# Performance work log

Measured on AMD Instinct MI355X. Metric: run time of the kernel, lower is better.

Reference implementation:

```python
import jax, jax.numpy as jnp
import numpy as np

N_GENES = 15135
K = int(np.ceil(0.5 * N_GENES))  # 7568, PyG TopKPooling ratio=0.5
BS, E, F_IN, H, HF, NC, L = 8, 242160, 64, 128, 512, 2, 3


def setup_inputs() -> dict:
    key = jax.random.key(0)
    ks = jax.random.split(key, 16)
    def lin(k, fin, fout):
        s = 1.0 / np.sqrt(fin)
        return jax.random.normal(k, (fin, fout), jnp.float32) * s
    x = jax.random.normal(ks[0], (BS, N_GENES, F_IN), jnp.float32)
    batch = jnp.zeros((BS,), jnp.int32)
    edge_index = jax.random.randint(ks[1], (2, E), 0, N_GENES, dtype=jnp.int32)
    CAT = L * H
    return {
        "x": x,
        "batch": batch,
        "edge_index": edge_index,
        "W1": lin(ks[2], F_IN, H), "b1": jnp.zeros((H,), jnp.float32),
        "W2": lin(ks[3], H, H),    "b2": jnp.zeros((H,), jnp.float32),
        "W3": lin(ks[4], H, H),    "b3": jnp.zeros((H,), jnp.float32),
        "topk_w": jax.random.normal(ks[5], (CAT,), jnp.float32) / np.sqrt(CAT),
        "fcW": lin(ks[6], CAT, 1), "fcb": jnp.zeros((1,), jnp.float32),
        "lin1W": lin(ks[7], K, HF), "lin1b": jnp.zeros((HF,), jnp.float32),
        "lin2W": lin(ks[8], HF, NC), "lin2b": jnp.zeros((NC,), jnp.float32),
    }


def reference(x, batch, edge_index, W1, b1, W2, b2, W3, b3,
              topk_w, fcW, fcb, lin1W, lin1b, lin2W, lin2b):
    bs = x.shape[0]
    # --- GCN normalization with self-loops (PyG GCNConv defaults) ---
    loop = jnp.arange(N_GENES, dtype=edge_index.dtype)
    src = jnp.concatenate([edge_index[0], loop])
    dst = jnp.concatenate([edge_index[1], loop])
    deg = jnp.zeros((N_GENES,), x.dtype).at[dst].add(1.0)
    dinv = jax.lax.rsqrt(deg)  # deg >= 1 due to self-loops
    norm = dinv[src] * dinv[dst]  # [E+N]

    def gcn(h, W, b):
        h = h @ W                                   # [bs, N, H]
        msg = h[:, src, :] * norm[None, :, None]    # gather + edge weight
        agg = jnp.zeros_like(h).at[:, dst, :].add(msg)  # scatter-add
        return agg + b

    h1 = jax.nn.relu(gcn(x, W1, b1))
    h2 = jax.nn.relu(gcn(h1, W2, b2))
    h3 = jax.nn.relu(gcn(h2, W3, b3))
    # mode='cat': stack on last dim then flatten -> feature order (H, layer)
    xc = jnp.stack([h1, h2, h3], -1).reshape(bs, N_GENES, -1)  # [bs, N, L*H]

    # --- TopKPooling (score = tanh(x.w/||w||), keep top ceil(0.5*N)) ---
    score = jnp.tanh((xc @ topk_w) / jnp.linalg.norm(topk_w))  # [bs, N]
    top_s, perm = jax.lax.top_k(score, K)                       # [bs, K]
    xp = jnp.take_along_axis(xc, perm[..., None], axis=1) * top_s[..., None]

    z = (xp @ fcW + fcb)[..., 0]          # [bs, K]
    h = jax.nn.relu(z @ lin1W + lin1b)    # [bs, HF]; dropout inactive (eval)
    logits = h @ lin2W + lin2b            # [bs, NC]
    return jax.nn.log_softmax(logits, axis=-1)
```

## Files before the change

kernel.cpp:

```cpp
#include <hip/hip_runtime.h>

#define N_G   15135
#define E_N   242160
#define BSZ   8
#define K_TOP 7568
#define NH    128
#define NBIN  65536
#define SUFS  65600

typedef float f4v __attribute__((ext_vector_type(4)));

__global__ void zero_kernel(int* __restrict__ p, int n) {
  int i = blockIdx.x * 1024 + threadIdx.x;
  if (i < n) p[i] = 0;
}

__global__ void count_kernel(const int* __restrict__ ei, int* __restrict__ cnt) {
  int e = blockIdx.x * 256 + threadIdx.x;
  if (e < E_N) atomicAdd(&cnt[ei[E_N + e]], 1);
}

__global__ __launch_bounds__(1024) void scan_kernel(const int* __restrict__ cnt,
                                                    int* __restrict__ rowstart,
                                                    float* __restrict__ dinv,
                                                    int4* __restrict__ rowdesc,
                                                    int* __restrict__ gctr,
                                                    const float* __restrict__ topk_w,
                                                    float* __restrict__ scal) {
  __shared__ int buf[1024];
  __shared__ int base;
  int tid = threadIdx.x;
  int i = blockIdx.x * 1024 + tid;
  int v = (i < N_G) ? cnt[i] : 0;
  float di = 1.0f / sqrtf((float)(v + 1));
  if (i < N_G) dinv[i] = di;
  buf[tid] = v;
  __syncthreads();
  for (int s = 1; s < 1024; s <<= 1) {
    int t = (tid >= s) ? buf[tid - s] : 0;
    __syncthreads();
    buf[tid] += t;
    __syncthreads();
  }
  if (tid == 1023) base = atomicAdd(gctr, buf[1023]);
  __syncthreads();
  if (i < N_G) {
    int rs = base + buf[tid] - v;
    rowstart[i] = rs;
    rowdesc[i] = make_int4(rs, v, __float_as_int(di), 0);
  }
  if (blockIdx.x == 0) {
    __shared__ float fbuf[512];
    if (tid < 512) {
      float w = (tid < 384) ? topk_w[tid] : 0.f;
      fbuf[tid] = w * w;
    }
    __syncthreads();
    for (int s = 256; s > 0; s >>= 1) {
      if (tid < s) fbuf[tid] += fbuf[tid + s];
      __syncthreads();
    }
    if (tid == 0) scal[0] = 1.0f / sqrtf(fbuf[0]);
  }
}

__global__ void fill_kernel(const int* __restrict__ ei, const int* __restrict__ rowstart,
                            const float* __restrict__ dinv, int* __restrict__ fillc,
                            int2* __restrict__ csr) {
  int e = blockIdx.x * 256 + threadIdx.x;
  if (e < E_N) {
    int s = ei[e], d = ei[E_N + e];
    int pos = rowstart[d] + atomicAdd(&fillc[d], 1);
    csr[pos] = make_int2(s, __float_as_int(dinv[s]));
  }
}

template<int CIN, bool BR>
__global__ __launch_bounds__(256, 6) void mm_kernel(const float* __restrict__ A,
                                                    const float* __restrict__ W,
                                                    const float* __restrict__ bias,
                                                    float* __restrict__ out) {
  __shared__ float Bst[32][132];
  __shared__ float Ast2[32][68];
  int tid = threadIdx.x;
  int b = blockIdx.x & 7;
  int ib = blockIdx.x >> 3;
  int rb0 = b * N_G + ib * 64;
  int rmax = N_G - ib * 64;
  int c0 = (tid & 31) * 4;
  int r0 = (tid >> 5) * 8;
  float acc[8][4];
#pragma unroll
  for (int i = 0; i < 8; i++)
#pragma unroll
    for (int j = 0; j < 4; j++) acc[i][j] = 0.f;

  for (int k0 = 0; k0 < CIN; k0 += 32) {
    {
      int koff = (tid & 7) * 4;
      int row = tid >> 3;
#pragma unroll
      for (int p = 0; p < 2; ++p) {
        int r = row + p * 32;
        f4v v = {0.f, 0.f, 0.f, 0.f};
        if (r < rmax) v = __builtin_nontemporal_load((const f4v*)(A + (size_t)(rb0 + r) * CIN + k0 + koff));
        Ast2[koff + 0][r] = v.x; Ast2[koff + 1][r] = v.y;
        Ast2[koff + 2][r] = v.z; Ast2[koff + 3][r] = v.w;
      }
    }
    {
      int cc = (tid & 31) * 4;
      int kr = tid >> 5;
#pragma unroll
      for (int p = 0; p < 4; ++p) {
        int k = kr + p * 8;
        *(float4*)&Bst[k][cc] = *(const float4*)(W + (size_t)(k0 + k) * NH + cc);
      }
    }
    __syncthreads();
#pragma unroll 4
    for (int kk = 0; kk < 32; ++kk) {
      float a[8], bb[4];
      *(float4*)&a[0] = *(const float4*)&Ast2[kk][r0];
      *(float4*)&a[4] = *(const float4*)&Ast2[kk][r0 + 4];
      *(float4*)&bb[0] = *(const float4*)&Bst[kk][c0];
#pragma unroll
      for (int i = 0; i < 8; i++)
#pragma unroll
        for (int j = 0; j < 4; j++)
          acc[i][j] = fmaf(a[i], bb[j], acc[i][j]);
    }
    __syncthreads();
  }
  float b0 = 0.f, b1 = 0.f, b2 = 0.f, b3 = 0.f;
  if (BR) { b0 = bias[c0]; b1 = bias[c0+1]; b2 = bias[c0+2]; b3 = bias[c0+3]; }
#pragma unroll
  for (int i = 0; i < 8; i++) {
    int r = r0 + i;
    if (r < rmax) {
      float4 v;
      if (BR) {
        v.x = fmaxf(acc[i][0] + b0, 0.f); v.y = fmaxf(acc[i][1] + b1, 0.f);
        v.z = fmaxf(acc[i][2] + b2, 0.f); v.w = fmaxf(acc[i][3] + b3, 0.f);
      } else {
        v.x = acc[i][0]; v.y = acc[i][1]; v.z = acc[i][2]; v.w = acc[i][3];
      }
      *(float4*)(out + (size_t)(rb0 + r) * NH + c0) = v;
    }
  }
}

template<int CH, bool BR>
__global__ __launch_bounds__(256) void agg_h_kernel(const float* __restrict__ src,
                                                    const int2* __restrict__ csr,
                                                    const int4* __restrict__ rowdesc,
                                                    const float* __restrict__ bias,
                                                    float* __restrict__ dst, int half) {
  int b = blockIdx.x & 7;
  int chunk = blockIdx.x >> 3;
  int wave = threadIdx.x >> 6, lane = threadIdx.x & 63;
  int d = chunk * 4 + wave;
  if (d >= N_G) return;
  d = __builtin_amdgcn_readfirstlane(d);
  int4 rd = rowdesc[d];
  int e0 = rd.x, n = rd.y;
  float dv = __int_as_float(rd.z);
  int c = (CH == 128) ? ((half << 6) + lane) : lane;
  const float* sb = src + (size_t)b * N_G * CH;
  const int2* ce = csr + e0;
  float acc[8];
  acc[0] = dv * sb[(size_t)d * CH + c];
#pragma unroll
  for (int k = 1; k < 8; ++k) acc[k] = 0.f;
  int l = 0;
  if (n >= 8) {
    int2 pA[8]; float vA[8];
#pragma unroll
    for (int k = 0; k < 8; ++k) pA[k] = ce[k];
#pragma unroll
    for (int k = 0; k < 8; ++k) vA[k] = sb[(size_t)pA[k].x * CH + c];
    l = 8;
    for (; l + 8 <= n; l += 8) {
      int2 pB[8]; float vB[8];
#pragma unroll
      for (int k = 0; k < 8; ++k) pB[k] = ce[l + k];
#pragma unroll
      for (int k = 0; k < 8; ++k) vB[k] = sb[(size_t)pB[k].x * CH + c];
#pragma unroll
      for (int k = 0; k < 8; ++k) acc[k] = fmaf(__int_as_float(pA[k].y), vA[k], acc[k]);
#pragma unroll
      for (int k = 0; k < 8; ++k) { pA[k] = pB[k]; vA[k] = vB[k]; }
    }
#pragma unroll
    for (int k = 0; k < 8; ++k) acc[k] = fmaf(__int_as_float(pA[k].y), vA[k], acc[k]);
  }
  for (; l < n; ++l) {
    int2 p = ce[l];
    acc[0] = fmaf(__int_as_float(p.y), sb[(size_t)p.x * CH + c], acc[0]);
  }
  float s = ((acc[0] + acc[1]) + (acc[2] + acc[3])) + ((acc[4] + acc[5]) + (acc[6] + acc[7]));
  float r = BR ? fmaxf(fmaf(dv, s, bias[c]), 0.f) : dv * s;
  __builtin_nontemporal_store(r, &dst[((size_t)b * N_G + d) * CH + c]);
}

__global__ __launch_bounds__(256) void agg_score_h_kernel(const float* __restrict__ hw,
                                                          const int2* __restrict__ csr,
                                                          const int4* __restrict__ rowdesc,
                                                          const float* __restrict__ bias,
                                                          const float* __restrict__ h1,
                                                          const float* __restrict__ h2,
                                                          const float* __restrict__ topk_w,
                                                          const float* __restrict__ fcW,
                                                          float* __restrict__ pd1,
                                                          float* __restrict__ pd2, int half) {
  int b = blockIdx.x & 7;
  int chunk = blockIdx.x >> 3;
  int wave = threadIdx.x >> 6, lane = threadIdx.x & 63;
  int d = chunk * 4 + wave;
  if (d >= N_G) return;
  d = __builtin_amdgcn_readfirstlane(d);
  int4 rd = rowdesc[d];
  int e0 = rd.x, n = rd.y;
  float dv = __int_as_float(rd.z);
  int c = (half << 6) + lane;
  const float* sb = hw + (size_t)b * N_G * NH;
  const int2* ce = csr + e0;
  size_t rbase = ((size_t)b * N_G + d) * NH + c;
  float u1 = __builtin_nontemporal_load(h1 + rbase);
  float u2 = __builtin_nontemporal_load(h2 + rbase);
  float acc[8];
  acc[0] = dv * sb[(size_t)d * NH + c];
#pragma unroll
  for (int k = 1; k < 8; ++k) acc[k] = 0.f;
  int l = 0;
  if (n >= 8) {
    int2 pA[8]; float vA[8];
#pragma unroll
    for (int k = 0; k < 8; ++k) pA[k] = ce[k];
#pragma unroll
    for (int k = 0; k < 8; ++k) vA[k] = sb[(size_t)pA[k].x * NH + c];
    l = 8;
    for (; l + 8 <= n; l += 8) {
      int2 pB[8]; float vB[8];
#pragma unroll
      for (int k = 0; k < 8; ++k) pB[k] = ce[l + k];
#pragma unroll
      for (int k = 0; k < 8; ++k) vB[k] = sb[(size_t)pB[k].x * NH + c];
#pragma unroll
      for (int k = 0; k < 8; ++k) acc[k] = fmaf(__int_as_float(pA[k].y), vA[k], acc[k]);
#pragma unroll
      for (int k = 0; k < 8; ++k) { pA[k] = pB[k]; vA[k] = vB[k]; }
    }
#pragma unroll
    for (int k = 0; k < 8; ++k) acc[k] = fmaf(__int_as_float(pA[k].y), vA[k], acc[k]);
  }
  for (; l < n; ++l) {
    int2 p = ce[l];
    acc[0] = fmaf(__int_as_float(p.y), sb[(size_t)p.x * NH + c], acc[0]);
  }
  float s = ((acc[0] + acc[1]) + (acc[2] + acc[3])) + ((acc[4] + acc[5]) + (acc[6] + acc[7]));
  float r = fmaxf(fmaf(dv, s, bias[c]), 0.f);
  float d1 = u1 * topk_w[c * 3] + u2 * topk_w[c * 3 + 1] + r * topk_w[c * 3 + 2];
  float d2 = u1 * fcW[c * 3]    + u2 * fcW[c * 3 + 1]    + r * fcW[c * 3 + 2];
#pragma unroll
  for (int sh = 32; sh > 0; sh >>= 1) {
    d1 += __shfl_down(d1, sh);
    d2 += __shfl_down(d2, sh);
  }
  if (lane == 0) {
    int gw = b * N_G + d;
    pd1[gw * 2 + half] = d1;
    pd2[gw * 2 + half] = d2;
  }
}

__global__ void combine_kernel(const float* __restrict__ pd1, const float* __restrict__ pd2,
                               const float* __restrict__ scal, float* __restrict__ score,
                               float* __restrict__ d2a, unsigned* __restrict__ keys,
                               int* __restrict__ hist) {
  int b = blockIdx.y;
  int i = blockIdx.x * 256 + threadIdx.x;
  if (i >= N_G) return;
  int gw = b * N_G + i;
  float d1 = pd1[2 * gw] + pd1[2 * gw + 1];
  float d2 = pd2[2 * gw] + pd2[2 * gw + 1];
  float sc = tanhf(d1 * scal[0]);
  score[gw] = sc;
  d2a[gw] = d2;
  unsigned u = __float_as_uint(sc);
  unsigned k32 = (u & 0x80000000u) ? ~u : (u | 0x80000000u);
  keys[gw] = k32;
  atomicAdd(&hist[b * NBIN + (int)(k32 >> 16)], 1);
}

__global__ __launch_bounds__(1024) void suffix_kernel(const int* __restrict__ hist,
                                                      int* __restrict__ suf) {
  __shared__ int buf[1024];
  int b = blockIdx.x;
  const int* hb = hist + b * NBIN;
  int* sb = suf + b * SUFS;
  int t = threadIdx.x;
  int base = t * 64;
  int s = 0;
  for (int k = 0; k < 64; ++k) s += hb[base + k];
  buf[t] = s;
  __syncthreads();
  for (int off = 1; off < 1024; off <<= 1) {
    int v = (t + off < 1024) ? buf[t + off] : 0;
    __syncthreads();
    buf[t] += v;
    __syncthreads();
  }
  int acc = buf[t] - s;
  if (t == 0) sb[NBIN] = 0;
  for (int k = 63; k >= 0; --k) {
    acc += hb[base + k];
    sb[base + k] = acc;
  }
}

__global__ void scatter_kernel(const unsigned* __restrict__ keys, int* __restrict__ hist,
                               const int* __restrict__ suf, int2* __restrict__ bucket) {
  int b = blockIdx.y;
  int i = blockIdx.x * 256 + threadIdx.x;
  if (i >= N_G) return;
  unsigned k = keys[b * N_G + i];
  int bin = (int)(k >> 16);
  int old = atomicSub(&hist[b * NBIN + bin], 1);
  int pos = suf[b * SUFS + bin + 1] + old - 1;
  bucket[b * N_G + pos] = make_int2((int)k, i);
}

__global__ void rank_z_kernel(const unsigned* __restrict__ keys, const int* __restrict__ suf,
                              const int2* __restrict__ bucket, const float* __restrict__ score,
                              const float* __restrict__ d2a, const float* __restrict__ fcb,
                              float* __restrict__ z) {
  int b = blockIdx.y;
  int i = blockIdx.x * 256 + threadIdx.x;
  if (i >= N_G) return;
  int gw = b * N_G + i;
  unsigned k = keys[gw];
  int bin = (int)(k >> 16);
  int lo = suf[b * SUFS + bin + 1];
  int hi = suf[b * SUFS + bin];
  int r = lo;
  const int2* bk = bucket + b * N_G;
  for (int p = lo; p < hi; ++p) {
    int2 e = bk[p];
    unsigned kj = (unsigned)e.x;
    r += (kj > k || (kj == k && e.y < i)) ? 1 : 0;
  }
  if (r < K_TOP) z[b * K_TOP + r] = fmaf(score[gw], d2a[gw], fcb[0]);
}

__global__ __launch_bounds__(256) void lin1_kernel(const float* __restrict__ z,
                                                   const float* __restrict__ W,
                                                   float* __restrict__ hpre) {
  __shared__ float zb[237];
  int b = blockIdx.y, rs = blockIdx.x;
  int r0 = rs * 237;
  int rn = K_TOP - r0; if (rn > 237) rn = 237;
  for (int q = threadIdx.x; q < rn; q += 256) zb[q] = z[b * K_TOP + r0 + q];
  __syncthreads();
  int c = threadIdx.x;
  float a0 = 0.f, a1 = 0.f;
  for (int r = 0; r < rn; ++r) {
    float zz = zb[r];
    const float* wr = W + (size_t)(r0 + r) * 512;
    a0 = fmaf(zz, wr[c], a0);
    a1 = fmaf(zz, wr[c + 256], a1);
  }
  atomicAdd(&hpre[b * 512 + c], a0);
  atomicAdd(&hpre[b * 512 + c + 256], a1);
}

__global__ __launch_bounds__(128) void lin2_kernel(const float* __restrict__ hpre,
                                                   const float* __restrict__ l1b,
                                                   const float* __restrict__ W2,
                                                   const float* __restrict__ l2b,
                                                   float* __restrict__ out) {
  int b = blockIdx.x, tid = threadIdx.x;
  float a0 = 0.f, a1 = 0.f;
  for (int j = tid; j < 512; j += 128) {
    float t = fmaxf(hpre[b * 512 + j] + l1b[j], 0.f);
    a0 = fmaf(t, W2[j * 2 + 0], a0);
    a1 = fmaf(t, W2[j * 2 + 1], a1);
  }
#pragma unroll
  for (int s = 32; s > 0; s >>= 1) {
    a0 += __shfl_down(a0, s);
    a1 += __shfl_down(a1, s);
  }
  __shared__ float red[2][2];
  if ((tid & 63) == 0) { red[tid >> 6][0] = a0; red[tid >> 6][1] = a1; }
  __syncthreads();
  if (tid == 0) {
    float l0 = red[0][0] + red[1][0] + l2b[0];
    float l1 = red[0][1] + red[1][1] + l2b[1];
    float m = fmaxf(l0, l1);
    float lse = m + logf(expf(l0 - m) + expf(l1 - m));
    out[b * 2 + 0] = l0 - lse;
    out[b * 2 + 1] = l1 - lse;
  }
}

extern "C" void kernel_launch(void* const* d_in, const int* in_sizes, int n_in,
                              void* d_out, int out_size, void* d_ws, size_t ws_size,
                              hipStream_t stream) {
  const float* x   = (const float*)d_in[0];
  const int*   ei  = (const int*)d_in[2];
  const float* W1  = (const float*)d_in[3];
  const float* b1  = (const float*)d_in[4];
  const float* W2  = (const float*)d_in[5];
  const float* b2  = (const float*)d_in[6];
  const float* W3  = (const float*)d_in[7];
  const float* b3  = (const float*)d_in[8];
  const float* tkw = (const float*)d_in[9];
  const float* fcW = (const float*)d_in[10];
  const float* fcb = (const float*)d_in[11];
  const float* l1W = (const float*)d_in[12];
  const float* l1b = (const float*)d_in[13];
  const float* l2W = (const float*)d_in[14];
  const float* l2b = (const float*)d_in[15];
  float* out = (float*)d_out;

  char* ws = (char*)d_ws;
  size_t off = 0;
  auto alloc = [&](size_t bytes) {
    char* p = ws + off;
    off += (bytes + 255) & ~(size_t)255;
    return p;
  };
  int*   cnt   = (int*)alloc(15136 * 4);
  int*   fillc = (int*)alloc(15136 * 4);
  int*   gctr  = (int*)alloc(256);
  float* hpre  = (float*)alloc(4096 * 4);
  int*   hist  = (int*)alloc((size_t)BSZ * NBIN * 4);
  int*   rowstart = (int*)alloc(15136 * 4);
  float* dinv  = (float*)alloc(15136 * 4);
  int4*  rowdesc = (int4*)alloc(15136 * 16);
  float* scal  = (float*)alloc(64);
  float* z     = (float*)alloc((size_t)BSZ * K_TOP * 4);
  float* score = (float*)alloc(121088 * 4);
  float* d2a   = (float*)alloc(121088 * 4);
  unsigned* keys = (unsigned*)alloc(121088 * 4);
  int*   suf   = (int*)alloc((size_t)BSZ * SUFS * 4);
  int2*  bucket = (int2*)alloc(121088 * 8);
  float* pd1   = (float*)alloc(121088 * 2 * 4);
  float* pd2   = (float*)alloc(121088 * 2 * 4);
  int2*  csr   = (int2*)alloc((size_t)E_N * 8);
  float* ax = (float*)alloc((size_t)BSZ * N_G * 64 * 4);
  float* hw = (float*)alloc((size_t)BSZ * N_G * NH * 4);
  float* h1 = (float*)alloc((size_t)BSZ * N_G * NH * 4);
  float* h2 = (float*)alloc((size_t)BSZ * N_G * NH * 4);
  (void)ws_size; (void)in_sizes; (void)n_in; (void)out_size;

  int zero_n = (int)(((char*)rowstart - (char*)cnt) / 4);
  zero_kernel<<<(zero_n + 1023) / 1024, 1024, 0, stream>>>(cnt, zero_n);
  count_kernel<<<(E_N + 255) / 256, 256, 0, stream>>>(ei, cnt);
  scan_kernel<<<(N_G + 1023) / 1024, 1024, 0, stream>>>(cnt, rowstart, dinv, rowdesc, gctr, tkw, scal);
  fill_kernel<<<(E_N + 255) / 256, 256, 0, stream>>>(ei, rowstart, dinv, fillc, csr);

  dim3 mmg(8 * 237);
  int aggblocks = 8 * ((N_G + 3) / 4);

  agg_h_kernel<64, false><<<aggblocks, 256, 0, stream>>>(x, csr, rowdesc, nullptr, ax, 0);
  mm_kernel<64, true><<<mmg, 256, 0, stream>>>(ax, W1, b1, h1);
  mm_kernel<128, false><<<mmg, 256, 0, stream>>>(h1, W2, nullptr, hw);
  agg_h_kernel<128, true><<<aggblocks, 256, 0, stream>>>(hw, csr, rowdesc, b2, h2, 0);
  agg_h_kernel<128, true><<<aggblocks, 256, 0, stream>>>(hw, csr, rowdesc, b2, h2, 1);
  mm_kernel<128, false><<<mmg, 256, 0, stream>>>(h2, W3, nullptr, hw);
  agg_score_h_kernel<<<aggblocks, 256, 0, stream>>>(hw, csr, rowdesc, b3,
                                                    h1, h2, tkw, fcW, pd1, pd2, 0);
  agg_score_h_kernel<<<aggblocks, 256, 0, stream>>>(hw, csr, rowdesc, b3,
                                                    h1, h2, tkw, fcW, pd1, pd2, 1);

  dim3 ng((N_G + 255) / 256, BSZ);
  combine_kernel<<<ng, 256, 0, stream>>>(pd1, pd2, scal, score, d2a, keys, hist);
  suffix_kernel<<<BSZ, 1024, 0, stream>>>(hist, suf);
  scatter_kernel<<<ng, 256, 0, stream>>>(keys, hist, suf, bucket);
  rank_z_kernel<<<ng, 256, 0, stream>>>(keys, suf, bucket, score, d2a, fcb, z);

  dim3 l1g(32, BSZ);
  lin1_kernel<<<l1g, 256, 0, stream>>>(z, l1W, hpre);
  lin2_kernel<<<BSZ, 128, 0, stream>>>(hpre, l1b, l2W, l2b, out);
}
```

Baseline: 663.4 us.

## Merge half-channel aggregation passes into single float2 pass and fuse score combine

The 128-channel GCN aggregations previously ran as two launches, one per 64-channel half, each re-walking the CSR edge list. Now each lane gathers a float2 covering both halves in one pass, which halves the edge-index traffic and launch count and widens each gather. The score kernel also does the tanh, key and histogram work directly, so the partial-dot buffers and the combine kernel are removed. The trade-off is more registers per thread for the float2 accumulators and a different floating-point summation order.

```diff
diff --git a/kernel.cpp b/kernel.cpp
--- a/kernel.cpp
+++ b/kernel.cpp
@@ -9,6 +9,7 @@
 #define SUFS  65600
 
 typedef float f4v __attribute__((ext_vector_type(4)));
+typedef float f2v __attribute__((ext_vector_type(2)));
 
 __global__ void zero_kernel(int* __restrict__ p, int n) {
   int i = blockIdx.x * 1024 + threadIdx.x;
@@ -150,12 +151,10 @@
   }
 }
 
-template<int CH, bool BR>
-__global__ __launch_bounds__(256) void agg_h_kernel(const float* __restrict__ src,
+__global__ __launch_bounds__(256) void agg64_kernel(const float* __restrict__ src,
                                                     const int2* __restrict__ csr,
                                                     const int4* __restrict__ rowdesc,
-                                                    const float* __restrict__ bias,
-                                                    float* __restrict__ dst, int half) {
+                                                    float* __restrict__ dst) {
   int b = blockIdx.x & 7;
   int chunk = blockIdx.x >> 3;
   int wave = threadIdx.x >> 6, lane = threadIdx.x & 63;
@@ -165,11 +164,10 @@
   int4 rd = rowdesc[d];
   int e0 = rd.x, n = rd.y;
   float dv = __int_as_float(rd.z);
-  int c = (CH == 128) ? ((half << 6) + lane) : lane;
-  const float* sb = src + (size_t)b * N_G * CH;
+  const float* sb = src + (size_t)b * N_G * 64;
   const int2* ce = csr + e0;
   float acc[8];
-  acc[0] = dv * sb[(size_t)d * CH + c];
+  acc[0] = dv * sb[(size_t)d * 64 + lane];
 #pragma unroll
   for (int k = 1; k < 8; ++k) acc[k] = 0.f;
   int l = 0;
@@ -178,14 +176,14 @@
 #pragma unroll
     for (int k = 0; k < 8; ++k) pA[k] = ce[k];
 #pragma unroll
-    for (int k = 0; k < 8; ++k) vA[k] = sb[(size_t)pA[k].x * CH + c];
+    for (int k = 0; k < 8; ++k) vA[k] = sb[(size_t)pA[k].x * 64 + lane];
     l = 8;
     for (; l + 8 <= n; l += 8) {
       int2 pB[8]; float vB[8];
 #pragma unroll
       for (int k = 0; k < 8; ++k) pB[k] = ce[l + k];
 #pragma unroll
-      for (int k = 0; k < 8; ++k) vB[k] = sb[(size_t)pB[k].x * CH + c];
+      for (int k = 0; k < 8; ++k) vB[k] = sb[(size_t)pB[k].x * 64 + lane];
 #pragma unroll
       for (int k = 0; k < 8; ++k) acc[k] = fmaf(__int_as_float(pA[k].y), vA[k], acc[k]);
 #pragma unroll
@@ -196,23 +194,17 @@
   }
   for (; l < n; ++l) {
     int2 p = ce[l];
-    acc[0] = fmaf(__int_as_float(p.y), sb[(size_t)p.x * CH + c], acc[0]);
+    acc[0] = fmaf(__int_as_float(p.y), sb[(size_t)p.x * 64 + lane], acc[0]);
   }
   float s = ((acc[0] + acc[1]) + (acc[2] + acc[3])) + ((acc[4] + acc[5]) + (acc[6] + acc[7]));
-  float r = BR ? fmaxf(fmaf(dv, s, bias[c]), 0.f) : dv * s;
-  __builtin_nontemporal_store(r, &dst[((size_t)b * N_G + d) * CH + c]);
-}
-
-__global__ __launch_bounds__(256) void agg_score_h_kernel(const float* __restrict__ hw,
-                                                          const int2* __restrict__ csr,
-                                                          const int4* __restrict__ rowdesc,
-                                                          const float* __restrict__ bias,
-                                                          const float* __restrict__ h1,
-                                                          const float* __restrict__ h2,
-                                                          const float* __restrict__ topk_w,
-                                                          const float* __restrict__ fcW,
-                                                          float* __restrict__ pd1,
-                                                          float* __restrict__ pd2, int half) {
+  __builtin_nontemporal_store(dv * s, &dst[((size_t)b * N_G + d) * 64 + lane]);
+}
+
+__global__ __launch_bounds__(256) void agg_f2_kernel(const float* __restrict__ hw,
+                                                     const int2* __restrict__ csr,
+                                                     const int4* __restrict__ rowdesc,
+                                                     const float* __restrict__ bias,
+                                                     float* __restrict__ hout) {
   int b = blockIdx.x & 7;
   int chunk = blockIdx.x >> 3;
   int wave = threadIdx.x >> 6, lane = threadIdx.x & 63;
@@ -222,46 +214,141 @@
   int4 rd = rowdesc[d];
   int e0 = rd.x, n = rd.y;
   float dv = __int_as_float(rd.z);
-  int c = (half << 6) + lane;
-  const float* sb = hw + (size_t)b * N_G * NH;
+  const f2v* sb = (const f2v*)(hw + (size_t)b * N_G * NH);
   const int2* ce = csr + e0;
-  size_t rbase = ((size_t)b * N_G + d) * NH + c;
-  float u1 = __builtin_nontemporal_load(h1 + rbase);
-  float u2 = __builtin_nontemporal_load(h2 + rbase);
-  float acc[8];
-  acc[0] = dv * sb[(size_t)d * NH + c];
-#pragma unroll
-  for (int k = 1; k < 8; ++k) acc[k] = 0.f;
+  f2v self = sb[(size_t)d * 64 + lane];
+  float ax[4], ay[4];
+  ax[0] = dv * self.x; ay[0] = dv * self.y;
+#pragma unroll
+  for (int k = 1; k < 4; ++k) { ax[k] = 0.f; ay[k] = 0.f; }
   int l = 0;
   if (n >= 8) {
-    int2 pA[8]; float vA[8];
+    int2 pA[8]; f2v vA[8];
 #pragma unroll
     for (int k = 0; k < 8; ++k) pA[k] = ce[k];
 #pragma unroll
-    for (int k = 0; k < 8; ++k) vA[k] = sb[(size_t)pA[k].x * NH + c];
+    for (int k = 0; k < 8; ++k) vA[k] = sb[(size_t)pA[k].x * 64 + lane];
     l = 8;
     for (; l + 8 <= n; l += 8) {
-      int2 pB[8]; float vB[8];
+      int2 pB[8]; f2v vB[8];
 #pragma unroll
       for (int k = 0; k < 8; ++k) pB[k] = ce[l + k];
 #pragma unroll
-      for (int k = 0; k < 8; ++k) vB[k] = sb[(size_t)pB[k].x * NH + c];
-#pragma unroll
-      for (int k = 0; k < 8; ++k) acc[k] = fmaf(__int_as_float(pA[k].y), vA[k], acc[k]);
+      for (int k = 0; k < 8; ++k) vB[k] = sb[(size_t)pB[k].x * 64 + lane];
+#pragma unroll
+      for (int k = 0; k < 8; ++k) {
+        float w = __int_as_float(pA[k].y);
+        ax[k & 3] = fmaf(w, vA[k].x, ax[k & 3]);
+        ay[k & 3] = fmaf(w, vA[k].y, ay[k & 3]);
+      }
 #pragma unroll
       for (int k = 0; k < 8; ++k) { pA[k] = pB[k]; vA[k] = vB[k]; }
     }
 #pragma unroll
-    for (int k = 0; k < 8; ++k) acc[k] = fmaf(__int_as_float(pA[k].y), vA[k], acc[k]);
+    for (int k = 0; k < 8; ++k) {
+      float w = __int_as_float(pA[k].y);
+      ax[k & 3] = fmaf(w, vA[k].x, ax[k & 3]);
+      ay[k & 3] = fmaf(w, vA[k].y, ay[k & 3]);
+    }
   }
   for (; l < n; ++l) {
     int2 p = ce[l];
-    acc[0] = fmaf(__int_as_float(p.y), sb[(size_t)p.x * NH + c], acc[0]);
-  }
-  float s = ((acc[0] + acc[1]) + (acc[2] + acc[3])) + ((acc[4] + acc[5]) + (acc[6] + acc[7]));
-  float r = fmaxf(fmaf(dv, s, bias[c]), 0.f);
-  float d1 = u1 * topk_w[c * 3] + u2 * topk_w[c * 3 + 1] + r * topk_w[c * 3 + 2];
-  float d2 = u1 * fcW[c * 3]    + u2 * fcW[c * 3 + 1]    + r * fcW[c * 3 + 2];
+    f2v v = sb[(size_t)p.x * 64 + lane];
+    float w = __int_as_float(p.y);
+    ax[0] = fmaf(w, v.x, ax[0]); ay[0] = fmaf(w, v.y, ay[0]);
+  }
+  float sx = (ax[0] + ax[1]) + (ax[2] + ax[3]);
+  float sy = (ay[0] + ay[1]) + (ay[2] + ay[3]);
+  const f2v* bb2 = (const f2v*)bias;
+  f2v bb = bb2[lane];
+  f2v r;
+  r.x = fmaxf(fmaf(dv, sx, bb.x), 0.f);
+  r.y = fmaxf(fmaf(dv, sy, bb.y), 0.f);
+  __builtin_nontemporal_store(r, &((f2v*)hout)[((size_t)b * N_G + d) * 64 + lane]);
+}
+
+__global__ __launch_bounds__(256) void agg_score_f2_kernel(const float* __restrict__ hw,
+                                                           const int2* __restrict__ csr,
+                                                           const int4* __restrict__ rowdesc,
+                                                           const float* __restrict__ bias,
+                                                           const float* __restrict__ h1,
+                                                           const float* __restrict__ h2,
+                                                           const float* __restrict__ topk_w,
+                                                           const float* __restrict__ fcW,
+                                                           const float* __restrict__ scal,
+                                                           float* __restrict__ score,
+                                                           float* __restrict__ d2a,
+                                                           unsigned* __restrict__ keys,
+                                                           int* __restrict__ hist) {
+  int b = blockIdx.x & 7;
+  int chunk = blockIdx.x >> 3;
+  int wave = threadIdx.x >> 6, lane = threadIdx.x & 63;
+  int d = chunk * 4 + wave;
+  if (d >= N_G) return;
+  d = __builtin_amdgcn_readfirstlane(d);
+  int4 rd = rowdesc[d];
+  int e0 = rd.x, n = rd.y;
+  float dv = __int_as_float(rd.z);
+  const f2v* sb = (const f2v*)(hw + (size_t)b * N_G * NH);
+  const int2* ce = csr + e0;
+  size_t rbase = ((size_t)b * N_G + d) * 64 + lane;
+  f2v u1 = __builtin_nontemporal_load(&((const f2v*)h1)[rbase]);
+  f2v u2 = __builtin_nontemporal_load(&((const f2v*)h2)[rbase]);
+  f2v self = sb[(size_t)d * 64 + lane];
+  float ax[4], ay[4];
+  ax[0] = dv * self.x; ay[0] = dv * self.y;
+#pragma unroll
+  for (int k = 1; k < 4; ++k) { ax[k] = 0.f; ay[k] = 0.f; }
+  int l = 0;
+  if (n >= 8) {
+    int2 pA[8]; f2v vA[8];
+#pragma unroll
+    for (int k = 0; k < 8; ++k) pA[k] = ce[k];
+#pragma unroll
+    for (int k = 0; k < 8; ++k) vA[k] = sb[(size_t)pA[k].x * 64 + lane];
+    l = 8;
+    for (; l + 8 <= n; l += 8) {
+      int2 pB[8]; f2v vB[8];
+#pragma unroll
+      for (int k = 0; k < 8; ++k) pB[k] = ce[l + k];
+#pragma unroll
+      for (int k = 0; k < 8; ++k) vB[k] = sb[(size_t)pB[k].x * 64 + lane];
+#pragma unroll
+      for (int k = 0; k < 8; ++k) {
+        float w = __int_as_float(pA[k].y);
+        ax[k & 3] = fmaf(w, vA[k].x, ax[k & 3]);
+        ay[k & 3] = fmaf(w, vA[k].y, ay[k & 3]);
+      }
+#pragma unroll
+      for (int k = 0; k < 8; ++k) { pA[k] = pB[k]; vA[k] = vB[k]; }
+    }
+#pragma unroll
+    for (int k = 0; k < 8; ++k) {
+      float w = __int_as_float(pA[k].y);
+      ax[k & 3] = fmaf(w, vA[k].x, ax[k & 3]);
+      ay[k & 3] = fmaf(w, vA[k].y, ay[k & 3]);
+    }
+  }
+  for (; l < n; ++l) {
+    int2 p = ce[l];
+    f2v v = sb[(size_t)p.x * 64 + lane];
+    float w = __int_as_float(p.y);
+    ax[0] = fmaf(w, v.x, ax[0]); ay[0] = fmaf(w, v.y, ay[0]);
+  }
+  float sx = (ax[0] + ax[1]) + (ax[2] + ax[3]);
+  float sy = (ay[0] + ay[1]) + (ay[2] + ay[3]);
+  const f2v* bb2 = (const f2v*)bias;
+  f2v bb = bb2[lane];
+  float rx = fmaxf(fmaf(dv, sx, bb.x), 0.f);
+  float ry = fmaxf(fmaf(dv, sy, bb.y), 0.f);
+  const f2v* tw2 = (const f2v*)topk_w;
+  const f2v* fw2 = (const f2v*)fcW;
+  f2v ta = tw2[lane * 3 + 0], tb = tw2[lane * 3 + 1], tc = tw2[lane * 3 + 2];
+  f2v fa = fw2[lane * 3 + 0], fb = fw2[lane * 3 + 1], fc = fw2[lane * 3 + 2];
+  float d1 = u1.x * ta.x + u2.x * ta.y + rx * tb.x
+           + u1.y * tb.y + u2.y * tc.x + ry * tc.y;
+  float d2 = u1.x * fa.x + u2.x * fa.y + rx * fb.x
+           + u1.y * fb.y + u2.y * fc.x + ry * fc.y;
 #pragma unroll
   for (int sh = 32; sh > 0; sh >>= 1) {
     d1 += __shfl_down(d1, sh);
@@ -269,28 +356,14 @@
   }
   if (lane == 0) {
     int gw = b * N_G + d;
-    pd1[gw * 2 + half] = d1;
-    pd2[gw * 2 + half] = d2;
-  }
-}
-
-__global__ void combine_kernel(const float* __restrict__ pd1, const float* __restrict__ pd2,
-                               const float* __restrict__ scal, float* __restrict__ score,
-                               float* __restrict__ d2a, unsigned* __restrict__ keys,
-                               int* __restrict__ hist) {
-  int b = blockIdx.y;
-  int i = blockIdx.x * 256 + threadIdx.x;
-  if (i >= N_G) return;
-  int gw = b * N_G + i;
-  float d1 = pd1[2 * gw] + pd1[2 * gw + 1];
-  float d2 = pd2[2 * gw] + pd2[2 * gw + 1];
-  float sc = tanhf(d1 * scal[0]);
-  score[gw] = sc;
-  d2a[gw] = d2;
-  unsigned u = __float_as_uint(sc);
-  unsigned k32 = (u & 0x80000000u) ? ~u : (u | 0x80000000u);
-  keys[gw] = k32;
-  atomicAdd(&hist[b * NBIN + (int)(k32 >> 16)], 1);
+    float sc = tanhf(d1 * scal[0]);
+    score[gw] = sc;
+    d2a[gw] = d2;
+    unsigned u = __float_as_uint(sc);
+    unsigned k32 = (u & 0x80000000u) ? ~u : (u | 0x80000000u);
+    keys[gw] = k32;
+    atomicAdd(&hist[b * NBIN + (int)(k32 >> 16)], 1);
+  }
 }
 
 __global__ __launch_bounds__(1024) void suffix_kernel(const int* __restrict__ hist,
@@ -446,8 +519,6 @@
   unsigned* keys = (unsigned*)alloc(121088 * 4);
   int*   suf   = (int*)alloc((size_t)BSZ * SUFS * 4);
   int2*  bucket = (int2*)alloc(121088 * 8);
-  float* pd1   = (float*)alloc(121088 * 2 * 4);
-  float* pd2   = (float*)alloc(121088 * 2 * 4);
   int2*  csr   = (int2*)alloc((size_t)E_N * 8);
   float* ax = (float*)alloc((size_t)BSZ * N_G * 64 * 4);
   float* hw = (float*)alloc((size_t)BSZ * N_G * NH * 4);
@@ -464,19 +535,15 @@
   dim3 mmg(8 * 237);
   int aggblocks = 8 * ((N_G + 3) / 4);
 
-  agg_h_kernel<64, false><<<aggblocks, 256, 0, stream>>>(x, csr, rowdesc, nullptr, ax, 0);
+  agg64_kernel<<<aggblocks, 256, 0, stream>>>(x, csr, rowdesc, ax);
   mm_kernel<64, true><<<mmg, 256, 0, stream>>>(ax, W1, b1, h1);
   mm_kernel<128, false><<<mmg, 256, 0, stream>>>(h1, W2, nullptr, hw);
-  agg_h_kernel<128, true><<<aggblocks, 256, 0, stream>>>(hw, csr, rowdesc, b2, h2, 0);
-  agg_h_kernel<128, true><<<aggblocks, 256, 0, stream>>>(hw, csr, rowdesc, b2, h2, 1);
+  agg_f2_kernel<<<aggblocks, 256, 0, stream>>>(hw, csr, rowdesc, b2, h2);
   mm_kernel<128, false><<<mmg, 256, 0, stream>>>(h2, W3, nullptr, hw);
-  agg_score_h_kernel<<<aggblocks, 256, 0, stream>>>(hw, csr, rowdesc, b3,
-                                                    h1, h2, tkw, fcW, pd1, pd2, 0);
-  agg_score_h_kernel<<<aggblocks, 256, 0, stream>>>(hw, csr, rowdesc, b3,
-                                                    h1, h2, tkw, fcW, pd1, pd2, 1);
+  agg_score_f2_kernel<<<aggblocks, 256, 0, stream>>>(hw, csr, rowdesc, b3, h1, h2,
+                                                     tkw, fcW, scal, score, d2a, keys, hist);
 
   dim3 ng((N_G + 255) / 256, BSZ);
-  combine_kernel<<<ng, 256, 0, stream>>>(pd1, pd2, scal, score, d2a, keys, hist);
   suffix_kernel<<<BSZ, 1024, 0, stream>>>(hist, suf);
   scatter_kernel<<<ng, 256, 0, stream>>>(keys, hist, suf, bucket);
   rank_z_kernel<<<ng, 256, 0, stream>>>(keys, suf, bucket, score, d2a, fcb, z);
```

After: 615.1 us. 7.3% less time.

## Vectorize GCN aggregation with float4 gathers and fuse score/combine into last layer

Applied to the files above, without the earlier changes.

Rewrites the three aggregation kernels so each lane gathers a float4 and lanes split across edges (2 or 4 edges per wave step), reduced by cross-lane shuffles. The two half-column launches per 128-wide layer collapse into one, and the combine kernel is folded into the final aggregation, removing the pd1/pd2 partial buffers. The aim is fewer, wider memory transactions, fewer launches and less intermediate traffic. In exchange there is more per-edge index selection work, a cross-lane reduction, and half the lanes sitting idle during the epilogue.

```diff
diff --git a/kernel.cpp b/kernel.cpp
--- a/kernel.cpp
+++ b/kernel.cpp
@@ -150,12 +150,10 @@
   }
 }
 
-template<int CH, bool BR>
-__global__ __launch_bounds__(256) void agg_h_kernel(const float* __restrict__ src,
-                                                    const int2* __restrict__ csr,
-                                                    const int4* __restrict__ rowdesc,
-                                                    const float* __restrict__ bias,
-                                                    float* __restrict__ dst, int half) {
+__global__ __launch_bounds__(256) void agg64_f4_kernel(const float* __restrict__ src,
+                                                       const int2* __restrict__ csr,
+                                                       const int4* __restrict__ rowdesc,
+                                                       float* __restrict__ dst) {
   int b = blockIdx.x & 7;
   int chunk = blockIdx.x >> 3;
   int wave = threadIdx.x >> 6, lane = threadIdx.x & 63;
@@ -165,54 +163,77 @@
   int4 rd = rowdesc[d];
   int e0 = rd.x, n = rd.y;
   float dv = __int_as_float(rd.z);
-  int c = (CH == 128) ? ((half << 6) + lane) : lane;
-  const float* sb = src + (size_t)b * N_G * CH;
+  int eh = lane >> 4;
+  int q = lane & 15;
+  const f4v* sb = (const f4v*)(src + (size_t)b * N_G * 64);
   const int2* ce = csr + e0;
-  float acc[8];
-  acc[0] = dv * sb[(size_t)d * CH + c];
-#pragma unroll
-  for (int k = 1; k < 8; ++k) acc[k] = 0.f;
+  f4v acc0 = {0.f,0.f,0.f,0.f}, acc1 = {0.f,0.f,0.f,0.f};
+  int nfull = n >> 5;
   int l = 0;
-  if (n >= 8) {
-    int2 pA[8]; float vA[8];
-#pragma unroll
-    for (int k = 0; k < 8; ++k) pA[k] = ce[k];
-#pragma unroll
-    for (int k = 0; k < 8; ++k) vA[k] = sb[(size_t)pA[k].x * CH + c];
-    l = 8;
-    for (; l + 8 <= n; l += 8) {
-      int2 pB[8]; float vB[8];
-#pragma unroll
-      for (int k = 0; k < 8; ++k) pB[k] = ce[l + k];
-#pragma unroll
-      for (int k = 0; k < 8; ++k) vB[k] = sb[(size_t)pB[k].x * CH + c];
-#pragma unroll
-      for (int k = 0; k < 8; ++k) acc[k] = fmaf(__int_as_float(pA[k].y), vA[k], acc[k]);
-#pragma unroll
-      for (int k = 0; k < 8; ++k) { pA[k] = pB[k]; vA[k] = vB[k]; }
-    }
-#pragma unroll
-    for (int k = 0; k < 8; ++k) acc[k] = fmaf(__int_as_float(pA[k].y), vA[k], acc[k]);
-  }
-  for (; l < n; ++l) {
-    int2 p = ce[l];
-    acc[0] = fmaf(__int_as_float(p.y), sb[(size_t)p.x * CH + c], acc[0]);
-  }
-  float s = ((acc[0] + acc[1]) + (acc[2] + acc[3])) + ((acc[4] + acc[5]) + (acc[6] + acc[7]));
-  float r = BR ? fmaxf(fmaf(dv, s, bias[c]), 0.f) : dv * s;
-  __builtin_nontemporal_store(r, &dst[((size_t)b * N_G + d) * CH + c]);
-}
-
-__global__ __launch_bounds__(256) void agg_score_h_kernel(const float* __restrict__ hw,
-                                                          const int2* __restrict__ csr,
-                                                          const int4* __restrict__ rowdesc,
-                                                          const float* __restrict__ bias,
-                                                          const float* __restrict__ h1,
-                                                          const float* __restrict__ h2,
-                                                          const float* __restrict__ topk_w,
-                                                          const float* __restrict__ fcW,
-                                                          float* __restrict__ pd1,
-                                                          float* __restrict__ pd2, int half) {
+  for (int blk = 0; blk < nfull; ++blk, l += 32) {
+    int srcs[8]; float ws[8];
+#pragma unroll
+    for (int k = 0; k < 8; ++k) {
+      int eb = l + 4 * k;
+      int2 p0 = ce[eb], p1 = ce[eb+1], p2 = ce[eb+2], p3 = ce[eb+3];
+      int sA = (eh & 1) ? p1.x : p0.x;
+      int sB = (eh & 1) ? p3.x : p2.x;
+      srcs[k] = (eh & 2) ? sB : sA;
+      float wA = (eh & 1) ? __int_as_float(p1.y) : __int_as_float(p0.y);
+      float wB = (eh & 1) ? __int_as_float(p3.y) : __int_as_float(p2.y);
+      ws[k] = (eh & 2) ? wB : wA;
+    }
+    f4v v[8];
+#pragma unroll
+    for (int k = 0; k < 8; ++k) v[k] = sb[(size_t)srcs[k] * 16 + q];
+#pragma unroll
+    for (int k = 0; k < 8; ++k) {
+      if (k & 1) acc1 += ws[k] * v[k]; else acc0 += ws[k] * v[k];
+    }
+  }
+  int rem = n - l;
+  if (rem > 0) {
+#pragma unroll
+    for (int k = 0; k < 8; ++k) {
+      if (4 * k < rem) {
+        int eb = l + 4 * k;
+        int2 p0 = ce[eb];
+        int2 p1 = ce[(4*k+1 < rem) ? eb+1 : eb];
+        int2 p2 = ce[(4*k+2 < rem) ? eb+2 : eb];
+        int2 p3 = ce[(4*k+3 < rem) ? eb+3 : eb];
+        float w0 = __int_as_float(p0.y);
+        float w1 = (4*k+1 < rem) ? __int_as_float(p1.y) : 0.f;
+        float w2 = (4*k+2 < rem) ? __int_as_float(p2.y) : 0.f;
+        float w3 = (4*k+3 < rem) ? __int_as_float(p3.y) : 0.f;
+        int sA = (eh & 1) ? p1.x : p0.x;
+        int sB = (eh & 1) ? p3.x : p2.x;
+        int s = (eh & 2) ? sB : sA;
+        float wA = (eh & 1) ? w1 : w0;
+        float wB = (eh & 1) ? w3 : w2;
+        float w = (eh & 2) ? wB : wA;
+        f4v v = sb[(size_t)s * 16 + q];
+        acc0 += w * v;
+      }
+    }
+  }
+  f4v acc = acc0 + acc1;
+  acc.x += __shfl_xor(acc.x, 16); acc.y += __shfl_xor(acc.y, 16);
+  acc.z += __shfl_xor(acc.z, 16); acc.w += __shfl_xor(acc.w, 16);
+  acc.x += __shfl_xor(acc.x, 32); acc.y += __shfl_xor(acc.y, 32);
+  acc.z += __shfl_xor(acc.z, 32); acc.w += __shfl_xor(acc.w, 32);
+  if (eh == 0) {
+    f4v self = sb[(size_t)d * 16 + q];
+    f4v s = acc + dv * self;
+    f4v r = dv * s;
+    __builtin_nontemporal_store(r, &((f4v*)dst)[((size_t)b * N_G + d) * 16 + q]);
+  }
+}
+
+__global__ __launch_bounds__(256) void agg_f4_kernel(const float* __restrict__ hw,
+                                                     const int2* __restrict__ csr,
+                                                     const int4* __restrict__ rowdesc,
+                                                     const float* __restrict__ bias,
+                                                     float* __restrict__ hout) {
   int b = blockIdx.x & 7;
   int chunk = blockIdx.x >> 3;
   int wave = threadIdx.x >> 6, lane = threadIdx.x & 63;
@@ -222,75 +243,165 @@
   int4 rd = rowdesc[d];
   int e0 = rd.x, n = rd.y;
   float dv = __int_as_float(rd.z);
-  int c = (half << 6) + lane;
-  const float* sb = hw + (size_t)b * N_G * NH;
+  int eh = lane >> 5;
+  int q = lane & 31;
+  const f4v* sb = (const f4v*)(hw + (size_t)b * N_G * NH);
   const int2* ce = csr + e0;
-  size_t rbase = ((size_t)b * N_G + d) * NH + c;
-  float u1 = __builtin_nontemporal_load(h1 + rbase);
-  float u2 = __builtin_nontemporal_load(h2 + rbase);
-  float acc[8];
-  acc[0] = dv * sb[(size_t)d * NH + c];
-#pragma unroll
-  for (int k = 1; k < 8; ++k) acc[k] = 0.f;
+  f4v acc0 = {0.f,0.f,0.f,0.f}, acc1 = {0.f,0.f,0.f,0.f};
+  int nfull = n >> 4;
   int l = 0;
-  if (n >= 8) {
-    int2 pA[8]; float vA[8];
-#pragma unroll
-    for (int k = 0; k < 8; ++k) pA[k] = ce[k];
-#pragma unroll
-    for (int k = 0; k < 8; ++k) vA[k] = sb[(size_t)pA[k].x * NH + c];
-    l = 8;
-    for (; l + 8 <= n; l += 8) {
-      int2 pB[8]; float vB[8];
-#pragma unroll
-      for (int k = 0; k < 8; ++k) pB[k] = ce[l + k];
-#pragma unroll
-      for (int k = 0; k < 8; ++k) vB[k] = sb[(size_t)pB[k].x * NH + c];
-#pragma unroll
-      for (int k = 0; k < 8; ++k) acc[k] = fmaf(__int_as_float(pA[k].y), vA[k], acc[k]);
-#pragma unroll
-      for (int k = 0; k < 8; ++k) { pA[k] = pB[k]; vA[k] = vB[k]; }
-    }
-#pragma unroll
-    for (int k = 0; k < 8; ++k) acc[k] = fmaf(__int_as_float(pA[k].y), vA[k], acc[k]);
-  }
-  for (; l < n; ++l) {
-    int2 p = ce[l];
-    acc[0] = fmaf(__int_as_float(p.y), sb[(size_t)p.x * NH + c], acc[0]);
-  }
-  float s = ((acc[0] + acc[1]) + (acc[2] + acc[3])) + ((acc[4] + acc[5]) + (acc[6] + acc[7]));
-  float r = fmaxf(fmaf(dv, s, bias[c]), 0.f);
-  float d1 = u1 * topk_w[c * 3] + u2 * topk_w[c * 3 + 1] + r * topk_w[c * 3 + 2];
-  float d2 = u1 * fcW[c * 3]    + u2 * fcW[c * 3 + 1]    + r * fcW[c * 3 + 2];
-#pragma unroll
-  for (int sh = 32; sh > 0; sh >>= 1) {
-    d1 += __shfl_down(d1, sh);
-    d2 += __shfl_down(d2, sh);
-  }
-  if (lane == 0) {
-    int gw = b * N_G + d;
-    pd1[gw * 2 + half] = d1;
-    pd2[gw * 2 + half] = d2;
-  }
-}
-
-__global__ void combine_kernel(const float* __restrict__ pd1, const float* __restrict__ pd2,
-                               const float* __restrict__ scal, float* __restrict__ score,
-                               float* __restrict__ d2a, unsigned* __restrict__ keys,
-                               int* __restrict__ hist) {
-  int b = blockIdx.y;
-  int i = blockIdx.x * 256 + threadIdx.x;
-  if (i >= N_G) return;
-  int gw = b * N_G + i;
-  float d1 = pd1[2 * gw] + pd1[2 * gw + 1];
-  float d2 = pd2[2 * gw] + pd2[2 * gw + 1];
-  float sc = tanhf(d1 * scal[0]);
-  score[gw] = sc;
-  d2a[gw] = d2;
-  unsigned u = __float_as_uint(sc);
-  unsigned k32 = (u & 0x80000000u) ? ~u : (u | 0x80000000u);
-  keys[gw] = k32;
-  atomicAdd(&hist[b * NBIN + (int)(k32 >> 16)], 1);
+  for (int blk = 0; blk < nfull; ++blk, l += 16) {
+    int srcs[8]; float ws[8];
+#pragma unroll
+    for (int k = 0; k < 8; ++k) {
+      int2 pL = ce[l + 2*k], pH = ce[l + 2*k + 1];
+      srcs[k] = eh ? pH.x : pL.x;
+      ws[k] = eh ? __int_as_float(pH.y) : __int_as_float(pL.y);
+    }
+    f4v v[8];
+#pragma unroll
+    for (int k = 0; k < 8; ++k) v[k] = sb[(size_t)srcs[k] * 32 + q];
+#pragma unroll
+    for (int k = 0; k < 8; ++k) {
+      if (k & 1) acc1 += ws[k] * v[k]; else acc0 += ws[k] * v[k];
+    }
+  }
+  int rem = n - l;
+  if (rem > 0) {
+#pragma unroll
+    for (int k = 0; k < 8; ++k) {
+      if (2 * k < rem) {
+        int2 pL = ce[l + 2*k];
+        int2 pH = ce[(2*k + 1 < rem) ? l + 2*k + 1 : l + 2*k];
+        float wH = (2*k + 1 < rem) ? __int_as_float(pH.y) : 0.f;
+        int s = eh ? pH.x : pL.x;
+        float w = eh ? wH : __int_as_float(pL.y);
+        f4v v = sb[(size_t)s * 32 + q];
+        acc0 += w * v;
+      }
+    }
+  }
+  f4v acc = acc0 + acc1;
+  acc.x += __shfl_xor(acc.x, 32); acc.y += __shfl_xor(acc.y, 32);
+  acc.z += __shfl_xor(acc.z, 32); acc.w += __shfl_xor(acc.w, 32);
+  if (eh == 0) {
+    f4v self = sb[(size_t)d * 32 + q];
+    const f4v* bb4 = (const f4v*)bias;
+    f4v bb = bb4[q];
+    f4v s = acc + dv * self;
+    f4v r;
+    r.x = fmaxf(fmaf(dv, s.x, bb.x), 0.f);
+    r.y = fmaxf(fmaf(dv, s.y, bb.y), 0.f);
+    r.z = fmaxf(fmaf(dv, s.z, bb.z), 0.f);
+    r.w = fmaxf(fmaf(dv, s.w, bb.w), 0.f);
+    __builtin_nontemporal_store(r, &((f4v*)hout)[((size_t)b * N_G + d) * 32 + q]);
+  }
+}
+
+__global__ __launch_bounds__(256) void agg_score_f4_kernel(const float* __restrict__ hw,
+                                                           const int2* __restrict__ csr,
+                                                           const int4* __restrict__ rowdesc,
+                                                           const float* __restrict__ bias,
+                                                           const float* __restrict__ h1,
+                                                           const float* __restrict__ h2,
+                                                           const float* __restrict__ topk_w,
+                                                           const float* __restrict__ fcW,
+                                                           const float* __restrict__ scal,
+                                                           float* __restrict__ score,
+                                                           float* __restrict__ d2a,
+                                                           unsigned* __restrict__ keys,
+                                                           int* __restrict__ hist) {
+  int b = blockIdx.x & 7;
+  int chunk = blockIdx.x >> 3;
+  int wave = threadIdx.x >> 6, lane = threadIdx.x & 63;
+  int d = chunk * 4 + wave;
+  if (d >= N_G) return;
+  d = __builtin_amdgcn_readfirstlane(d);
+  int4 rd = rowdesc[d];
+  int e0 = rd.x, n = rd.y;
+  float dv = __int_as_float(rd.z);
+  int eh = lane >> 5;
+  int q = lane & 31;
+  const f4v* sb = (const f4v*)(hw + (size_t)b * N_G * NH);
+  const int2* ce = csr + e0;
+  size_t rbase = ((size_t)b * N_G + d) * 32 + q;
+  f4v u1 = __builtin_nontemporal_load(&((const f4v*)h1)[rbase]);
+  f4v u2 = __builtin_nontemporal_load(&((const f4v*)h2)[rbase]);
+  f4v acc0 = {0.f,0.f,0.f,0.f}, acc1 = {0.f,0.f,0.f,0.f};
+  int nfull = n >> 4;
+  int l = 0;
+  for (int blk = 0; blk < nfull; ++blk, l += 16) {
+    int srcs[8]; float ws[8];
+#pragma unroll
+    for (int k = 0; k < 8; ++k) {
+      int2 pL = ce[l + 2*k], pH = ce[l + 2*k + 1];
+      srcs[k] = eh ? pH.x : pL.x;
+      ws[k] = eh ? __int_as_float(pH.y) : __int_as_float(pL.y);
+    }
+    f4v v[8];
+#pragma unroll
+    for (int k = 0; k < 8; ++k) v[k] = sb[(size_t)srcs[k] * 32 + q];
+#pragma unroll
+    for (int k = 0; k < 8; ++k) {
+      if (k & 1) acc1 += ws[k] * v[k]; else acc0 += ws[k] * v[k];
+    }
+  }
+  int rem = n - l;
+  if (rem > 0) {
+#pragma unroll
+    for (int k = 0; k < 8; ++k) {
+      if (2 * k < rem) {
+        int2 pL = ce[l + 2*k];
+        int2 pH = ce[(2*k + 1 < rem) ? l + 2*k + 1 : l + 2*k];
+        float wH = (2*k + 1 < rem) ? __int_as_float(pH.y) : 0.f;
+        int s = eh ? pH.x : pL.x;
+        float w = eh ? wH : __int_as_float(pL.y);
+        f4v v = sb[(size_t)s * 32 + q];
+        acc0 += w * v;
+      }
+    }
+  }
+  f4v acc = acc0 + acc1;
+  acc.x += __shfl_xor(acc.x, 32); acc.y += __shfl_xor(acc.y, 32);
+  acc.z += __shfl_xor(acc.z, 32); acc.w += __shfl_xor(acc.w, 32);
+  if (eh == 0) {
+    f4v self = sb[(size_t)d * 32 + q];
+    const f4v* bb4 = (const f4v*)bias;
+    f4v bb = bb4[q];
+    f4v s = acc + dv * self;
+    f4v r;
+    r.x = fmaxf(fmaf(dv, s.x, bb.x), 0.f);
+    r.y = fmaxf(fmaf(dv, s.y, bb.y), 0.f);
+    r.z = fmaxf(fmaf(dv, s.z, bb.z), 0.f);
+    r.w = fmaxf(fmaf(dv, s.w, bb.w), 0.f);
+    const f4v* tw4 = (const f4v*)topk_w;
+    const f4v* fw4 = (const f4v*)fcW;
+    f4v t0 = tw4[q*3+0], t1 = tw4[q*3+1], t2 = tw4[q*3+2];
+    f4v f0 = fw4[q*3+0], f1 = fw4[q*3+1], f2 = fw4[q*3+2];
+    float d1 = u1.x * t0.x + u2.x * t0.y + r.x * t0.z
+             + u1.y * t0.w + u2.y * t1.x + r.y * t1.y
+             + u1.z * t1.z + u2.z * t1.w + r.z * t2.x
+             + u1.w * t2.y + u2.w * t2.z + r.w * t2.w;
+    float d2 = u1.x * f0.x + u2.x * f0.y + r.x * f0.z
+             + u1.y * f0.w + u2.y * f1.x + r.y * f1.y
+             + u1.z * f1.z + u2.z * f1.w + r.z * f2.x
+             + u1.w * f2.y + u2.w * f2.z + r.w * f2.w;
+#pragma unroll
+    for (int sh = 16; sh > 0; sh >>= 1) {
+      d1 += __shfl_down(d1, sh, 32);
+      d2 += __shfl_down(d2, sh, 32);
+    }
+    if (q == 0) {
+      int gw = b * N_G + d;
+      float sc = tanhf(d1 * scal[0]);
+      score[gw] = sc;
+      d2a[gw] = d2;
+      unsigned u = __float_as_uint(sc);
+      unsigned k32 = (u & 0x80000000u) ? ~u : (u | 0x80000000u);
+      keys[gw] = k32;
+      atomicAdd(&hist[b * NBIN + (int)(k32 >> 16)], 1);
+    }
+  }
 }
 
 __global__ __launch_bounds__(1024) void suffix_kernel(const int* __restrict__ hist,
@@ -446,8 +557,6 @@
   unsigned* keys = (unsigned*)alloc(121088 * 4);
   int*   suf   = (int*)alloc((size_t)BSZ * SUFS * 4);
   int2*  bucket = (int2*)alloc(121088 * 8);
-  float* pd1   = (float*)alloc(121088 * 2 * 4);
-  float* pd2   = (float*)alloc(121088 * 2 * 4);
   int2*  csr   = (int2*)alloc((size_t)E_N * 8);
   float* ax = (float*)alloc((size_t)BSZ * N_G * 64 * 4);
   float* hw = (float*)alloc((size_t)BSZ * N_G * NH * 4);
@@ -464,19 +573,15 @@
   dim3 mmg(8 * 237);
   int aggblocks = 8 * ((N_G + 3) / 4);
 
-  agg_h_kernel<64, false><<<aggblocks, 256, 0, stream>>>(x, csr, rowdesc, nullptr, ax, 0);
+  agg64_f4_kernel<<<aggblocks, 256, 0, stream>>>(x, csr, rowdesc, ax);
   mm_kernel<64, true><<<mmg, 256, 0, stream>>>(ax, W1, b1, h1);
   mm_kernel<128, false><<<mmg, 256, 0, stream>>>(h1, W2, nullptr, hw);
-  agg_h_kernel<128, true><<<aggblocks, 256, 0, stream>>>(hw, csr, rowdesc, b2, h2, 0);
-  agg_h_kernel<128, true><<<aggblocks, 256, 0, stream>>>(hw, csr, rowdesc, b2, h2, 1);
+  agg_f4_kernel<<<aggblocks, 256, 0, stream>>>(hw, csr, rowdesc, b2, h2);
   mm_kernel<128, false><<<mmg, 256, 0, stream>>>(h2, W3, nullptr, hw);
-  agg_score_h_kernel<<<aggblocks, 256, 0, stream>>>(hw, csr, rowdesc, b3,
-                                                    h1, h2, tkw, fcW, pd1, pd2, 0);
-  agg_score_h_kernel<<<aggblocks, 256, 0, stream>>>(hw, csr, rowdesc, b3,
-                                                    h1, h2, tkw, fcW, pd1, pd2, 1);
+  agg_score_f4_kernel<<<aggblocks, 256, 0, stream>>>(hw, csr, rowdesc, b3, h1, h2,
+                                                     tkw, fcW, scal, score, d2a, keys, hist);
 
   dim3 ng((N_G + 255) / 256, BSZ);
-  combine_kernel<<<ng, 256, 0, stream>>>(pd1, pd2, scal, score, d2a, keys, hist);
   suffix_kernel<<<BSZ, 1024, 0, stream>>>(hist, suf);
   scatter_kernel<<<ng, 256, 0, stream>>>(keys, hist, suf, bucket);
   rank_z_kernel<<<ng, 256, 0, stream>>>(keys, suf, bucket, score, d2a, fcb, z);
```

Result: faster. 624.9 us (-5.8%).
